# Kernel optimization log

Hardware: AMD Instinct MI355X
Metric: run time of the kernel (lower is better)

## Reference

```python
import jax, jax.numpy as jnp
import numpy as np


def setup_inputs() -> dict:
    key = jax.random.key(0)
    k1, k2 = jax.random.split(key)
    hidden = jax.random.normal(k1, (32, 4096, 768), dtype=jnp.float32)
    querys = jax.random.normal(k2, (1, 768), dtype=jnp.float32)
    return {"hidden": hidden, "querys": querys}


def reference(hidden, querys):
    # scores: [B, S] = hidden @ querys^T (single query)
    scores = jnp.einsum("bsh,qh->bsq", hidden, querys)[..., 0]  # [B, S]
    attn = jax.nn.softmax(scores, axis=-1)                      # [B, S]
    # weighted sum over sequence: [B, H]
    result = jnp.einsum("bs,bsh->bh", attn, hidden)
    return result
```

## Files before the change

kernel.cpp:

```cpp
#include <hip/hip_runtime.h>
#include <math.h>

#define BATCH 32
#define SEQ   4096
#define HID   768
#define HV4   (HID / 4)
#define CHUNKS 64
#define ROWS_PER_BLOCK (SEQ / CHUNKS)
#define NWAVES 4
#define ROWS_PER_WAVE (ROWS_PER_BLOCK / NWAVES)
#define RGROUP 4

__device__ __forceinline__ float dot4(float4 a, float4 b) {
  return a.x * b.x + a.y * b.y + a.z * b.z + a.w * b.w;
}

__global__ __launch_bounds__(256, 4)
void attn_pass1(const float* __restrict__ hidden,
                const float* __restrict__ q,
                float* __restrict__ m_ws,
                float* __restrict__ l_ws,
                float* __restrict__ o_ws) {
  const int chunk = blockIdx.x;
  const int b     = blockIdx.y;
  const int tid   = threadIdx.x;
  const int wave  = tid >> 6;
  const int lane  = tid & 63;

  const float4* q4 = reinterpret_cast<const float4*>(q);
  const float4 qa = q4[lane];
  const float4 qb = q4[lane + 64];
  const float4 qc = q4[lane + 128];

  float m = -INFINITY;
  float l = 0.0f;
  float4 oa = make_float4(0.f, 0.f, 0.f, 0.f);
  float4 ob = make_float4(0.f, 0.f, 0.f, 0.f);
  float4 oc = make_float4(0.f, 0.f, 0.f, 0.f);

  const int row0 = chunk * ROWS_PER_BLOCK + wave * ROWS_PER_WAVE;
  const float4* base = reinterpret_cast<const float4*>(hidden)
                     + ((size_t)b * SEQ + (size_t)row0) * HV4;

  for (int g = 0; g < ROWS_PER_WAVE; g += RGROUP) {
    float4 ra[RGROUP], rb[RGROUP], rc[RGROUP];
    #pragma unroll
    for (int r = 0; r < RGROUP; ++r) {
      const float4* rp = base + (size_t)(g + r) * HV4;
      ra[r] = rp[lane];
      rb[r] = rp[lane + 64];
      rc[r] = rp[lane + 128];
    }

    float pd[RGROUP];
    #pragma unroll
    for (int r = 0; r < RGROUP; ++r)
      pd[r] = dot4(ra[r], qa) + dot4(rb[r], qb) + dot4(rc[r], qc);

    #pragma unroll
    for (int off = 32; off >= 1; off >>= 1) {
      #pragma unroll
      for (int r = 0; r < RGROUP; ++r)
        pd[r] += __shfl_xor(pd[r], off, 64);
    }

    const float gm = fmaxf(fmaxf(pd[0], pd[1]), fmaxf(pd[2], pd[3]));
    if (gm > m) {
      const float a = __expf(m - gm);
      l *= a;
      oa.x *= a; oa.y *= a; oa.z *= a; oa.w *= a;
      ob.x *= a; ob.y *= a; ob.z *= a; ob.w *= a;
      oc.x *= a; oc.y *= a; oc.z *= a; oc.w *= a;
      m = gm;
    }

    float p[RGROUP];
    #pragma unroll
    for (int r = 0; r < RGROUP; ++r) {
      p[r] = __expf(pd[r] - m);
      l += p[r];
    }
    #pragma unroll
    for (int r = 0; r < RGROUP; ++r) {
      oa.x += p[r] * ra[r].x; oa.y += p[r] * ra[r].y;
      oa.z += p[r] * ra[r].z; oa.w += p[r] * ra[r].w;
      ob.x += p[r] * rb[r].x; ob.y += p[r] * rb[r].y;
      ob.z += p[r] * rb[r].z; ob.w += p[r] * rb[r].w;
      oc.x += p[r] * rc[r].x; oc.y += p[r] * rc[r].y;
      oc.z += p[r] * rc[r].z; oc.w += p[r] * rc[r].w;
    }
  }

  __shared__ float s_o[NWAVES][HID];
  __shared__ float s_m[NWAVES];
  __shared__ float s_l[NWAVES];
  float4* so4 = reinterpret_cast<float4*>(s_o[wave]);
  so4[lane]       = oa;
  so4[lane + 64]  = ob;
  so4[lane + 128] = oc;
  if (lane == 0) { s_m[wave] = m; s_l[wave] = l; }
  __syncthreads();

  const float mb = fmaxf(fmaxf(s_m[0], s_m[1]), fmaxf(s_m[2], s_m[3]));
  const float a0 = __expf(s_m[0] - mb);
  const float a1 = __expf(s_m[1] - mb);
  const float a2 = __expf(s_m[2] - mb);
  const float a3 = __expf(s_m[3] - mb);
  const float lb = a0 * s_l[0] + a1 * s_l[1] + a2 * s_l[2] + a3 * s_l[3];

  const int pidx = b * CHUNKS + chunk;
  float* O = o_ws + (size_t)pidx * HID;
  #pragma unroll
  for (int j = 0; j < 3; ++j) {
    const int h = tid + 256 * j;
    O[h] = a0 * s_o[0][h] + a1 * s_o[1][h] + a2 * s_o[2][h] + a3 * s_o[3][h];
  }
  if (tid == 0) { m_ws[pidx] = mb; l_ws[pidx] = lb; }
}

__global__ __launch_bounds__(256)
void attn_pass2(const float* __restrict__ m_ws,
                const float* __restrict__ l_ws,
                const float* __restrict__ o_ws,
                float* __restrict__ out) {
  const int b   = blockIdx.x;
  const int tid = threadIdx.x;

  float mg = -INFINITY;
  for (int c = 0; c < CHUNKS; ++c)
    mg = fmaxf(mg, m_ws[b * CHUNKS + c]);

  float L = 0.0f;
  float acc0 = 0.f, acc1 = 0.f, acc2 = 0.f;
  for (int c = 0; c < CHUNKS; ++c) {
    const int pidx = b * CHUNKS + c;
    const float a = __expf(m_ws[pidx] - mg);
    L += a * l_ws[pidx];
    const float* O = o_ws + (size_t)pidx * HID;
    acc0 += a * O[tid];
    acc1 += a * O[tid + 256];
    acc2 += a * O[tid + 512];
  }
  const float inv = 1.0f / L;
  out[(size_t)b * HID + tid]       = acc0 * inv;
  out[(size_t)b * HID + tid + 256] = acc1 * inv;
  out[(size_t)b * HID + tid + 512] = acc2 * inv;
}

extern "C" void kernel_launch(void* const* d_in, const int* in_sizes, int n_in,
                              void* d_out, int out_size, void* d_ws, size_t ws_size,
                              hipStream_t stream) {
  const float* hidden = (const float*)d_in[0];
  const float* q      = (const float*)d_in[1];
  float* out = (float*)d_out;

  float* m_ws = (float*)d_ws;
  float* l_ws = m_ws + BATCH * CHUNKS;
  float* o_ws = l_ws + BATCH * CHUNKS;

  dim3 grid1(CHUNKS, BATCH);
  attn_pass1<<<grid1, 256, 0, stream>>>(hidden, q, m_ws, l_ws, o_ws);
  attn_pass2<<<BATCH, 256, 0, stream>>>(m_ws, l_ws, o_ws, out);
}
```

Before: 532.1 us.

## Fuse split-softmax combine into main kernel via last-block atomic counter

The separate reduction kernel is removed. Each block bumps a per-batch atomic counter after writing its partial results, and the last block to finish for a batch performs the cross-chunk softmax merge and writes the output. CHUNKS is halved from 64 to 32, which doubles the rows each block processes and halves the partial data to merge. This saves a kernel launch and gap, but it adds a memset launch, threadfence/atomic overhead, and a serialized tail in the last block. The smaller grid of 1024 blocks may also reduce latency hiding when streaming hidden from HBM.

```diff
diff --git a/kernel.cpp b/kernel.cpp
--- a/kernel.cpp
+++ b/kernel.cpp
@@ -5,7 +5,7 @@
 #define SEQ   4096
 #define HID   768
 #define HV4   (HID / 4)
-#define CHUNKS 64
+#define CHUNKS 32
 #define ROWS_PER_BLOCK (SEQ / CHUNKS)
 #define NWAVES 4
 #define ROWS_PER_WAVE (ROWS_PER_BLOCK / NWAVES)
@@ -16,11 +16,13 @@
 }
 
 __global__ __launch_bounds__(256, 4)
-void attn_pass1(const float* __restrict__ hidden,
+void attn_fused(const float* __restrict__ hidden,
                 const float* __restrict__ q,
+                int* __restrict__ cnt,
                 float* __restrict__ m_ws,
                 float* __restrict__ l_ws,
-                float* __restrict__ o_ws) {
+                float* __restrict__ o_ws,
+                float* __restrict__ out) {
   const int chunk = blockIdx.x;
   const int b     = blockIdx.y;
   const int tid   = threadIdx.x;
@@ -94,6 +96,7 @@
   __shared__ float s_o[NWAVES][HID];
   __shared__ float s_m[NWAVES];
   __shared__ float s_l[NWAVES];
+  __shared__ int s_last;
   float4* so4 = reinterpret_cast<float4*>(s_o[wave]);
   so4[lane]       = oa;
   so4[lane + 64]  = ob;
@@ -116,15 +119,17 @@
     O[h] = a0 * s_o[0][h] + a1 * s_o[1][h] + a2 * s_o[2][h] + a3 * s_o[3][h];
   }
   if (tid == 0) { m_ws[pidx] = mb; l_ws[pidx] = lb; }
-}
 
-__global__ __launch_bounds__(256)
-void attn_pass2(const float* __restrict__ m_ws,
-                const float* __restrict__ l_ws,
-                const float* __restrict__ o_ws,
-                float* __restrict__ out) {
-  const int b   = blockIdx.x;
-  const int tid = threadIdx.x;
+  __syncthreads();
+  if (tid == 0) {
+    __threadfence();
+    const int old = atomicAdd(&cnt[b], 1);
+    s_last = (old == CHUNKS - 1);
+  }
+  __syncthreads();
+  if (!s_last) return;
+
+  __threadfence();
 
   float mg = -INFINITY;
   for (int c = 0; c < CHUNKS; ++c)
@@ -133,13 +138,13 @@
   float L = 0.0f;
   float acc0 = 0.f, acc1 = 0.f, acc2 = 0.f;
   for (int c = 0; c < CHUNKS; ++c) {
-    const int pidx = b * CHUNKS + c;
-    const float a = __expf(m_ws[pidx] - mg);
-    L += a * l_ws[pidx];
-    const float* O = o_ws + (size_t)pidx * HID;
-    acc0 += a * O[tid];
-    acc1 += a * O[tid + 256];
-    acc2 += a * O[tid + 512];
+    const int pi = b * CHUNKS + c;
+    const float a = __expf(m_ws[pi] - mg);
+    L += a * l_ws[pi];
+    const float* Oc = o_ws + (size_t)pi * HID;
+    acc0 += a * Oc[tid];
+    acc1 += a * Oc[tid + 256];
+    acc2 += a * Oc[tid + 512];
   }
   const float inv = 1.0f / L;
   out[(size_t)b * HID + tid]       = acc0 * inv;
@@ -154,11 +159,13 @@
   const float* q      = (const float*)d_in[1];
   float* out = (float*)d_out;
 
-  float* m_ws = (float*)d_ws;
+  int*   cnt  = (int*)d_ws;
+  float* m_ws = (float*)d_ws + 32;
   float* l_ws = m_ws + BATCH * CHUNKS;
   float* o_ws = l_ws + BATCH * CHUNKS;
 
-  dim3 grid1(CHUNKS, BATCH);
-  attn_pass1<<<grid1, 256, 0, stream>>>(hidden, q, m_ws, l_ws, o_ws);
-  attn_pass2<<<BATCH, 256, 0, stream>>>(m_ws, l_ws, o_ws, out);
+  hipMemsetAsync(cnt, 0, BATCH * sizeof(int), stream);
+
+  dim3 grid(CHUNKS, BATCH);
+  attn_fused<<<grid, 256, 0, stream>>>(hidden, q, cnt, m_ws, l_ws, o_ws, out);
 }
```

Result: slower. 600.5 us (+12.9%).
